# Kernel tuning notes

Hardware: AMD Instinct MI355X
Metric: run time of the kernel (lower is better)

Reference implementation:

```python
import jax, jax.numpy as jnp
import numpy as np

N0, N1, N2 = 100000, 25000, 6250
E0, E1, E2 = 600000, 150000, 37500
K = 6


def cheb_conv(x, edge_index, W, b):
    """torch_geometric ChebConv with sym normalization, lambda_max=2:
    L_hat = -D^{-1/2} A D^{-1/2}; T0=x, T1=L_hat x, Tk=2 L_hat T_{k-1} - T_{k-2}."""
    n = x.shape[0]
    src, dst = edge_index[0], edge_index[1]
    deg = jax.ops.segment_sum(jnp.ones(src.shape[0], x.dtype), src, num_segments=n)
    dinv = jnp.where(deg > 0, jax.lax.rsqrt(jnp.maximum(deg, 1.0)), 0.0)
    w = -(dinv[src] * dinv[dst])  # [E]

    def prop(h):  # (L_hat h)_i = sum_{j->i} w_ij h_j
        return jax.ops.segment_sum(w[:, None] * h[src], dst, num_segments=n)

    Tx0 = x
    out = Tx0 @ W[0]
    Tx1 = prop(x)
    out = out + Tx1 @ W[1]
    for k in range(2, W.shape[0]):
        Tx2 = 2.0 * prop(Tx1) - Tx0
        out = out + Tx2 @ W[k]
        Tx0, Tx1 = Tx1, Tx2
    return out + b


def pool(x, rows, cols, vals, n_out):
    # sparse.mm(D, x): y[r] += v * x[c]
    return jax.ops.segment_sum(vals[:, None] * x[cols], rows, num_segments=n_out)


def setup_inputs() -> dict:
    key = jax.random.key(0)
    ks = jax.random.split(key, 16)
    inp = {}
    inp["x"] = jax.random.normal(ks[0], (N0, 3), jnp.float32)
    inp["edge_index0"] = jax.random.randint(ks[1], (2, E0), 0, N0, jnp.int32)
    inp["edge_index1"] = jax.random.randint(ks[2], (2, E1), 0, N1, jnp.int32)
    inp["edge_index2"] = jax.random.randint(ks[3], (2, E2), 0, N2, jnp.int32)
    s = 0.05
    inp["W0"] = jax.random.normal(ks[4], (K, 3, 128), jnp.float32) * s
    inp["b0"] = jax.random.normal(ks[5], (128,), jnp.float32) * s
    inp["W1"] = jax.random.normal(ks[6], (K, 128, 128), jnp.float32) * s
    inp["b1"] = jax.random.normal(ks[7], (128,), jnp.float32) * s
    inp["W2"] = jax.random.normal(ks[8], (K, 128, 256), jnp.float32) * s
    inp["b2"] = jax.random.normal(ks[9], (256,), jnp.float32) * s
    inp["D0_rows"] = jax.random.randint(ks[10], (100000,), 0, N1, jnp.int32)
    inp["D0_cols"] = jax.random.randint(ks[11], (100000,), 0, N0, jnp.int32)
    inp["D0_vals"] = jax.random.uniform(ks[12], (100000,), jnp.float32)
    inp["D1_rows"] = jax.random.randint(ks[13], (25000,), 0, N2, jnp.int32)
    inp["D1_cols"] = jax.random.randint(ks[14], (25000,), 0, N1, jnp.int32)
    inp["D1_vals"] = jax.random.uniform(ks[15], (25000,), jnp.float32)
    k2 = jax.random.split(jax.random.fold_in(key, 1), 2)
    inp["linW"] = jax.random.normal(k2[0], (10, N2 * 256), jnp.float32) * 0.001
    inp["linb"] = jax.random.normal(k2[1], (10,), jnp.float32) * s
    return inp


def reference(x, edge_index0, edge_index1, edge_index2, W0, b0, W1, b1, W2, b2,
              D0_rows, D0_cols, D0_vals, D1_rows, D1_cols, D1_vals, linW, linb):
    h = jax.nn.relu(cheb_conv(x, edge_index0, W0, b0))      # [N0,128]
    h = pool(h, D0_rows, D0_cols, D0_vals, N1)               # [N1,128]
    h = jax.nn.relu(cheb_conv(h, edge_index1, W1, b1))      # [N1,128]
    h = pool(h, D1_rows, D1_cols, D1_vals, N2)               # [N2,128]
    h = cheb_conv(h, edge_index2, W2, b2)                    # [N2,256]
    Z = linW @ h.reshape(-1) + linb                           # [10]
    return Z
```

## Files before the change

### kernel.cpp

```cpp
#include <hip/hip_runtime.h>


namespace {
constexpr int cN0 = 100000, cN1 = 25000, cN2 = 6250;
constexpr int cE0 = 600000, cE1 = 150000, cE2 = 37500;
constexpr int cD  = cN2 * 256;

constexpr int JN[8]  = {cN0, cN1, cN2, cN1, cN2, cN0, cN1, cN2};
constexpr int JE[8]  = {cE0, cE1, cE2, 100000, 25000, cE0, cE1, cE2};
constexpr int JB[8]  = {391, 98, 25, 98, 25, 391, 98, 25};
constexpr int JBBASE[9] = {0, 391, 489, 514, 612, 637, 1028, 1126, 1151};
constexpr int TB = 1151;
constexpr int JCB[8] = {293, 74, 19, 49, 13, 293, 74, 19};
constexpr int JCBASE[9] = {0, 293, 367, 386, 435, 448, 741, 815, 834};
constexpr int TCB = 834;
constexpr int CHUNK = 2048;
constexpr int BSTRIDE = 400;

constexpr int EBASE[5]   = {0, 600000, 750000, 787500, 887500};
constexpr int E_TOTAL    = 912500;
constexpr int SBASE[3]   = {0, 600000, 750000};
constexpr int S_TOTAL    = 787500;
constexpr int NBASE[5]   = {0, 100096, 125184, 131584, 156672};
constexpr int NPAD_TOTAL = 163072;
constexpr int DEGBASE[3] = {0, 100000, 125000};
constexpr int DEG_TOTAL  = 131250;
}

typedef __attribute__((ext_vector_type(8))) short short8;
typedef __attribute__((ext_vector_type(4))) float floatx4;

__device__ inline ushort f2bf(float f) {
  union { float f; unsigned u; } v; v.f = f;
  unsigned u = v.u;
  return (ushort)((u + 0x7FFFu + ((u >> 16) & 1u)) >> 16);
}

__device__ inline int job_of_cb(int cb) {
  int j = 0;
  while (cb >= JCBASE[j + 1]) ++j;
  return j;
}
__device__ inline int job_of_bucket(int g) {
  int j = 0;
  while (g >= JBBASE[j + 1]) ++j;
  return j;
}

__global__ __launch_bounds__(256) void c1_count_kernel(
    const int* __restrict__ k0, const int* __restrict__ k1, const int* __restrict__ k2,
    const int* __restrict__ k3, const int* __restrict__ k4, const int* __restrict__ k5,
    const int* __restrict__ k6, const int* __restrict__ k7,
    int* __restrict__ cntCB) {
  __shared__ int cnt[BSTRIDE];
  int cb = blockIdx.x;
  int j = job_of_cb(cb);
  int lb = cb - JCBASE[j];
  const int* keys;
  switch (j) {
    case 0: keys = k0; break; case 1: keys = k1; break; case 2: keys = k2; break;
    case 3: keys = k3; break; case 4: keys = k4; break; case 5: keys = k5; break;
    case 6: keys = k6; break; default: keys = k7; break;
  }
  int nB = JB[j];
  for (int b = threadIdx.x; b < nB; b += 256) cnt[b] = 0;
  __syncthreads();
  int e0 = lb * CHUNK;
  int e1 = min(e0 + CHUNK, JE[j]);
  for (int e = e0 + threadIdx.x; e < e1; e += 256)
    atomicAdd(&cnt[keys[e] >> 8], 1);
  __syncthreads();
  for (int b = threadIdx.x; b < nB; b += 256)
    cntCB[cb * BSTRIDE + b] = cnt[b];
}

__global__ __launch_bounds__(256) void c2a_scan_kernel(int* __restrict__ cntCB,
                                                       int* __restrict__ bucketTot) {
  __shared__ int s[256];
  int g = blockIdx.x;
  int j = job_of_bucket(g);
  int b = g - JBBASE[j];
  int cb0 = JCBASE[j], nCB = JCB[j];
  int carry = 0;
  for (int c0 = 0; c0 < nCB; c0 += 256) {
    int i = c0 + threadIdx.x;
    int v = (i < nCB) ? cntCB[(cb0 + i) * BSTRIDE + b] : 0;
    s[threadIdx.x] = v;
    __syncthreads();
    for (int d = 1; d < 256; d <<= 1) {
      int t = (threadIdx.x >= d) ? s[threadIdx.x - d] : 0;
      __syncthreads();
      s[threadIdx.x] += t;
      __syncthreads();
    }
    if (i < nCB) cntCB[(cb0 + i) * BSTRIDE + b] = carry + s[threadIdx.x] - v;
    carry += s[255];
    __syncthreads();
  }
  if (threadIdx.x == 0) bucketTot[g] = carry;
}

__global__ __launch_bounds__(256) void c2b_scan_kernel(const int* __restrict__ bucketTot,
                                                       int* __restrict__ bucketBase) {
  __shared__ int s[256];
  int j = blockIdx.x;
  int g0 = JBBASE[j], nB = JB[j];
  int carry = 0;
  for (int c0 = 0; c0 < nB; c0 += 256) {
    int i = c0 + threadIdx.x;
    int v = (i < nB) ? bucketTot[g0 + i] : 0;
    s[threadIdx.x] = v;
    __syncthreads();
    for (int d = 1; d < 256; d <<= 1) {
      int t = (threadIdx.x >= d) ? s[threadIdx.x - d] : 0;
      __syncthreads();
      s[threadIdx.x] += t;
      __syncthreads();
    }
    if (i < nB) bucketBase[g0 + i] = carry + s[threadIdx.x] - v;
    carry += s[255];
    __syncthreads();
  }
}

__global__ __launch_bounds__(256) void c3_src_kernel(
    const int* __restrict__ s0, const int* __restrict__ s1, const int* __restrict__ s2,
    const int* __restrict__ cntCB, const int* __restrict__ bucketBase,
    int* __restrict__ scatSrc) {
  __shared__ int base[BSTRIDE];
  int cb = blockIdx.x + JCBASE[5];
  int j = job_of_cb(cb);
  int lb = cb - JCBASE[j];
  const int* keys = (j == 5) ? s0 : (j == 6) ? s1 : s2;
  int nB = JB[j];
  for (int b = threadIdx.x; b < nB; b += 256)
    base[b] = SBASE[j - 5] + bucketBase[JBBASE[j] + b] + cntCB[cb * BSTRIDE + b];
  __syncthreads();
  int e0 = lb * CHUNK;
  int e1 = min(e0 + CHUNK, JE[j]);
  for (int e = e0 + threadIdx.x; e < e1; e += 256) {
    int s = keys[e];
    int pos = atomicAdd(&base[s >> 8], 1);
    scatSrc[pos] = s & 255;
  }
}

__global__ __launch_bounds__(256) void ddeg_kernel(const int* __restrict__ scatSrc,
                                                   const int* __restrict__ bucketTot,
                                                   const int* __restrict__ bucketBase,
                                                   float* __restrict__ dinv) {
  __shared__ int cnt[256];
  int g = blockIdx.x + JBBASE[5];
  int j = job_of_bucket(g);
  int b = g - JBBASE[j];
  int st = SBASE[j - 5] + bucketBase[g];
  int en = st + bucketTot[g];
  cnt[threadIdx.x] = 0;
  __syncthreads();
  for (int idx = st + threadIdx.x; idx < en; idx += 256)
    atomicAdd(&cnt[scatSrc[idx]], 1);
  __syncthreads();
  int node = b * 256 + threadIdx.x;
  if (node < JN[j]) {
    int c = cnt[threadIdx.x];
    dinv[DEGBASE[j - 5] + node] = (c > 0) ? rsqrtf((float)c) : 0.f;
  }
}

__global__ __launch_bounds__(256) void c3_dst_kernel(
    const int* __restrict__ d0, const int* __restrict__ s0,
    const int* __restrict__ d1, const int* __restrict__ s1,
    const int* __restrict__ d2, const int* __restrict__ s2,
    const int* __restrict__ p0r, const int* __restrict__ p0c, const float* __restrict__ p0v,
    const int* __restrict__ p1r, const int* __restrict__ p1c, const float* __restrict__ p1v,
    const float* __restrict__ dinv,
    const int* __restrict__ cntCB, const int* __restrict__ bucketBase,
    int2* __restrict__ scatPairs) {
  __shared__ int base[BSTRIDE];
  int cb = blockIdx.x;
  int j = job_of_cb(cb);
  int lb = cb - JCBASE[j];
  const int* dk; const int* sk; const float* vv = nullptr;
  switch (j) {
    case 0: dk = d0; sk = s0; break;
    case 1: dk = d1; sk = s1; break;
    case 2: dk = d2; sk = s2; break;
    case 3: dk = p0r; sk = p0c; vv = p0v; break;
    default: dk = p1r; sk = p1c; vv = p1v; break;
  }
  int nB = JB[j];
  for (int b = threadIdx.x; b < nB; b += 256)
    base[b] = EBASE[j] + bucketBase[JBBASE[j] + b] + cntCB[cb * BSTRIDE + b];
  __syncthreads();
  int e0 = lb * CHUNK;
  int e1 = min(e0 + CHUNK, JE[j]);
  for (int e = e0 + threadIdx.x; e < e1; e += 256) {
    int d = dk[e];
    int s = sk[e];
    float w;
    if (j < 3) w = -(dinv[DEGBASE[j] + s] * dinv[DEGBASE[j] + d]);
    else w = vv[e];
    int pos = atomicAdd(&base[d >> 8], 1);
    scatPairs[pos] = make_int2(((d & 255) << 17) | s, __float_as_int(w));
  }
}

__global__ __launch_bounds__(256) void dcsr_kernel(const int2* __restrict__ scatPairs,
                                                   const int* __restrict__ bucketTot,
                                                   const int* __restrict__ bucketBase,
                                                   int* __restrict__ off,
                                                   int2* __restrict__ csrPairs) {
  __shared__ int cnt[256];
  __shared__ int sArr[256];
  __shared__ int cur[256];
  int g = blockIdx.x;
  int j = job_of_bucket(g);
  int b = g - JBBASE[j];
  int relBase = bucketBase[g];
  int st = EBASE[j] + relBase;
  int en = st + bucketTot[g];
  cnt[threadIdx.x] = 0;
  __syncthreads();
  for (int idx = st + threadIdx.x; idx < en; idx += 256)
    atomicAdd(&cnt[scatPairs[idx].x >> 17], 1);
  __syncthreads();
  int v = cnt[threadIdx.x];
  sArr[threadIdx.x] = v;
  __syncthreads();
  for (int d = 1; d < 256; d <<= 1) {
    int t = (threadIdx.x >= d) ? sArr[threadIdx.x - d] : 0;
    __syncthreads();
    sArr[threadIdx.x] += t;
    __syncthreads();
  }
  int excl = sArr[threadIdx.x] - v;
  int node = b * 256 + threadIdx.x;
  if (node < JN[j]) off[NBASE[j] + node] = relBase + excl;
  if (threadIdx.x == 0 && b == JB[j] - 1) off[NBASE[j] + JN[j]] = JE[j];
  cur[threadIdx.x] = st + excl;
  __syncthreads();
  for (int idx = st + threadIdx.x; idx < en; idx += 256) {
    int2 p = scatPairs[idx];
    int dl = p.x >> 17;
    int s = p.x & 0x1FFFF;
    int pos = atomicAdd(&cur[dl], 1);
    csrPairs[pos] = make_int2(s, p.y);
  }
}

__global__ __launch_bounds__(256) void csr_prop128_kernel(
    const int* __restrict__ off, const int2* __restrict__ pairs,
    const float* __restrict__ h, float* __restrict__ y, ushort* __restrict__ ybf,
    const float* __restrict__ prev, float scale, int N) {
  int r = blockIdx.x * 8 + (threadIdx.x >> 5);
  int l = threadIdx.x & 31;
  if (r >= N) return;
  int s = off[r], e = off[r + 1];
  const float4* h4 = (const float4*)h;
  float ax = 0.f, ay = 0.f, az = 0.f, aw = 0.f;
  int j = s;
  for (; j + 2 <= e; j += 2) {
    int2 p0 = pairs[j];
    int2 p1 = pairs[j + 1];
    float4 v0 = h4[(size_t)p0.x * 32 + l];
    float4 v1 = h4[(size_t)p1.x * 32 + l];
    float w0 = __int_as_float(p0.y);
    float w1 = __int_as_float(p1.y);
    ax += w0 * v0.x + w1 * v1.x;
    ay += w0 * v0.y + w1 * v1.y;
    az += w0 * v0.z + w1 * v1.z;
    aw += w0 * v0.w + w1 * v1.w;
  }
  if (j < e) {
    int2 p = pairs[j];
    float4 v0 = h4[(size_t)p.x * 32 + l];
    float w = __int_as_float(p.y);
    ax += w * v0.x; ay += w * v0.y; az += w * v0.z; aw += w * v0.w;
  }
  float4 v = make_float4(scale * ax, scale * ay, scale * az, scale * aw);
  if (prev) {
    float4 pv = ((const float4*)prev)[(size_t)r * 32 + l];
    v.x -= pv.x; v.y -= pv.y; v.z -= pv.z; v.w -= pv.w;
  }
  ((float4*)y)[(size_t)r * 32 + l] = v;
  uint2 sp = make_uint2(f2bf(v.x) | ((unsigned)f2bf(v.y) << 16),
                        f2bf(v.z) | ((unsigned)f2bf(v.w) << 16));
  ((uint2*)ybf)[(size_t)r * 32 + l] = sp;
}

__global__ void csr_prop3_kernel(const int* __restrict__ off, const int2* __restrict__ pairs,
                                 const float4* __restrict__ h, float4* __restrict__ y,
                                 const float4* __restrict__ prev, float scale, int N) {
  int r = blockIdx.x * blockDim.x + threadIdx.x;
  if (r >= N) return;
  int s = off[r], e = off[r + 1];
  float ax = 0.f, ay = 0.f, az = 0.f;
  int j = s;
  for (; j + 4 <= e; j += 4) {
    int2 p0 = pairs[j], p1 = pairs[j + 1], p2 = pairs[j + 2], p3 = pairs[j + 3];
    float4 h0 = h[p0.x], h1 = h[p1.x], h2 = h[p2.x], h3 = h[p3.x];
    float w0 = __int_as_float(p0.y), w1 = __int_as_float(p1.y);
    float w2 = __int_as_float(p2.y), w3 = __int_as_float(p3.y);
    ax += w0 * h0.x + w1 * h1.x + w2 * h2.x + w3 * h3.x;
    ay += w0 * h0.y + w1 * h1.y + w2 * h2.y + w3 * h3.y;
    az += w0 * h0.z + w1 * h1.z + w2 * h2.z + w3 * h3.z;
  }
  for (; j < e; ++j) {
    int2 p = pairs[j];
    float4 hv = h[p.x];
    float w = __int_as_float(p.y);
    ax += w * hv.x; ay += w * hv.y; az += w * hv.z;
  }
  float4 v = make_float4(scale * ax, scale * ay, scale * az, 0.f);
  if (prev) {
    float4 pv = prev[r];
    v.x -= pv.x; v.y -= pv.y; v.z -= pv.z;
  }
  y[r] = v;
}

__global__ void copyx_kernel(const float* __restrict__ x, float4* __restrict__ Tb, int N) {
  int r = blockIdx.x * 256 + threadIdx.x;
  if (r < N) Tb[r] = make_float4(x[3 * r], x[3 * r + 1], x[3 * r + 2], 0.f);
}

__global__ __launch_bounds__(256) void g18pool_kernel(
    const int* __restrict__ off, const int2* __restrict__ pairs,
    const float4* __restrict__ Tb0, const float* __restrict__ W0,
    const float* __restrict__ b0, float* __restrict__ T0out,
    ushort* __restrict__ T0bf, int N, int N0) {
  int r = blockIdx.x * 2 + (threadIdx.x >> 7);
  int f = threadIdx.x & 127;
  float wcol[18];
#pragma unroll
  for (int t = 0; t < 18; ++t) wcol[t] = W0[t * 128 + f];
  float bv = b0[f];
  if (r >= N) return;
  int s = off[r], e = off[r + 1];
  float acc = 0.f;
  for (int j = s; j < e; ++j) {
    int2 p = pairs[j];
    float v = __int_as_float(p.y);
    float d = bv;
#pragma unroll
    for (int k = 0; k < 6; ++k) {
      float4 t = Tb0[(size_t)k * N0 + p.x];
      d += t.x * wcol[k * 3 + 0] + t.y * wcol[k * 3 + 1] + t.z * wcol[k * 3 + 2];
    }
    acc += v * fmaxf(d, 0.f);
  }
  T0out[(size_t)r * 128 + f] = acc;
  T0bf[(size_t)r * 128 + f] = f2bf(acc);
}

__global__ void prep_w_kernel(const float* __restrict__ W1, const float* __restrict__ W2,
                              ushort* __restrict__ Wt1, ushort* __restrict__ Wt2) {
  int i = blockIdx.x * 256 + threadIdx.x;
  if (i < 768 * 128) {
    int k = i / 128, n = i - k * 128;
    Wt1[(size_t)n * 768 + k] = f2bf(W1[i]);
  } else {
    int i2 = i - 768 * 128;
    if (i2 < 768 * 256) {
      int k = i2 / 256, n = i2 - k * 256;
      Wt2[(size_t)n * 768 + k] = f2bf(W2[i2]);
    }
  }
}

template <int RELU>
__global__ __launch_bounds__(256, 2) void gemm_mfma_kernel(
    const ushort* __restrict__ Tbf, const ushort* __restrict__ Wt,
    const float* __restrict__ bias, float* __restrict__ C, int M, int N) {
  __shared__ ushort Al[64][40];
  __shared__ ushort Bl[128][40];
  const int tid = threadIdx.x;
  const int rowBase = blockIdx.x * 64;
  const int colBase = blockIdx.y * 128;
  const int wave = tid >> 6;
  const int lane = tid & 63;
  const int m16 = lane & 15;
  const int quad = lane >> 4;
  const size_t Mstride = (size_t)M * 128;

  floatx4 acc[8];
#pragma unroll
  for (int c = 0; c < 8; ++c)
#pragma unroll
    for (int r = 0; r < 4; ++r) acc[c][r] = 0.f;

  const int sRow = tid >> 2;
  const int sK8 = (tid & 3) * 8;
  const int growA = rowBase + sRow;
  const bool aValid = growA < M;

  for (int kc = 0; kc < 24; ++kc) {
    uint4 av = make_uint4(0, 0, 0, 0);
    if (aValid)
      av = *(const uint4*)(Tbf + (size_t)(kc >> 2) * Mstride + (size_t)growA * 128
                           + ((kc & 3) << 5) + sK8);
    *(uint4*)&Al[sRow][sK8] = av;
#pragma unroll
    for (int l = 0; l < 2; ++l) {
      int lin = tid + l * 256;
      int bRow = lin >> 2;
      int bK8 = (lin & 3) * 8;
      *(uint4*)&Bl[bRow][bK8] =
          *(const uint4*)(Wt + (size_t)(colBase + bRow) * 768 + kc * 32 + bK8);
    }
    __syncthreads();

    short8 a = *(const short8*)&Al[wave * 16 + m16][quad * 8];
#pragma unroll
    for (int c = 0; c < 8; ++c) {
      short8 b = *(const short8*)&Bl[c * 16 + m16][quad * 8];
      acc[c] = __builtin_amdgcn_mfma_f32_16x16x32_bf16(a, b, acc[c], 0, 0, 0);
    }
    __syncthreads();
  }

#pragma unroll
  for (int c = 0; c < 8; ++c) {
    int col = colBase + c * 16 + m16;
    float bv = bias[col];
#pragma unroll
    for (int r = 0; r < 4; ++r) {
      int row = rowBase + wave * 16 + quad * 4 + r;
      if (row < M) {
        float v = acc[c][r] + bv;
        if (RELU) v = fmaxf(v, 0.f);
        C[(size_t)row * N + col] = v;
      }
    }
  }
}

__global__ void initout_kernel(float* __restrict__ out, const float* __restrict__ linb) {
  int i = threadIdx.x;
  if (i < 10) out[i] = linb[i];
}

__global__ __launch_bounds__(256) void linear_kernel(const float* __restrict__ Wl,
                                                     const float* __restrict__ h,
                                                     float* __restrict__ out, int D) {
  float p[10];
#pragma unroll
  for (int j = 0; j < 10; ++j) p[j] = 0.f;
  int stride = gridDim.x * blockDim.x;
  for (int i = blockIdx.x * blockDim.x + threadIdx.x; i < D; i += stride) {
    float hv = h[i];
#pragma unroll
    for (int j = 0; j < 10; ++j) p[j] += Wl[(size_t)j * D + i] * hv;
  }
#pragma unroll
  for (int j = 0; j < 10; ++j) {
#pragma unroll
    for (int off = 32; off > 0; off >>= 1) p[j] += __shfl_down(p[j], off, 64);
  }
  __shared__ float s[4][10];
  int wave = threadIdx.x >> 6, lane = threadIdx.x & 63;
  if (lane == 0) {
#pragma unroll
    for (int j = 0; j < 10; ++j) s[wave][j] = p[j];
  }
  __syncthreads();
  if (threadIdx.x < 10) {
    float t = s[0][threadIdx.x] + s[1][threadIdx.x] + s[2][threadIdx.x] + s[3][threadIdx.x];
    atomicAdd(&out[threadIdx.x], t);
  }
}

extern "C" void kernel_launch(void* const* d_in, const int* in_sizes, int n_in,
                              void* d_out, int out_size, void* d_ws, size_t ws_size,
                              hipStream_t stream) {
  const float* x    = (const float*)d_in[0];
  const int*   ei0  = (const int*)d_in[1];
  const int*   ei1  = (const int*)d_in[2];
  const int*   ei2  = (const int*)d_in[3];
  const float* W0   = (const float*)d_in[4];
  const float* b0   = (const float*)d_in[5];
  const float* W1   = (const float*)d_in[6];
  const float* b1   = (const float*)d_in[7];
  const float* W2   = (const float*)d_in[8];
  const float* b2   = (const float*)d_in[9];
  const int*   D0r  = (const int*)d_in[10];
  const int*   D0c  = (const int*)d_in[11];
  const float* D0v  = (const float*)d_in[12];
  const int*   D1r  = (const int*)d_in[13];
  const int*   D1c  = (const int*)d_in[14];
  const float* D1v  = (const float*)d_in[15];
  const float* linW = (const float*)d_in[16];
  const float* linb = (const float*)d_in[17];
  float* out = (float*)d_out;
  (void)in_sizes; (void)n_in; (void)out_size; (void)ws_size;

  const int* src0 = ei0;            const int* dst0 = ei0 + cE0;
  const int* src1 = ei1;            const int* dst1 = ei1 + cE1;
  const int* src2 = ei2;            const int* dst2 = ei2 + cE2;

  float* ws = (float*)d_ws;
  size_t off = 0;
  auto alloc = [&](size_t n) {
    float* p = ws + off;
    off += (n + 63) & ~size_t(63);
    return p;
  };
  float* dinv       = alloc(DEG_TOTAL);
  int*   cntCB      = (int*)alloc((size_t)TCB * BSTRIDE);
  int*   bucketTot  = (int*)alloc(TB);
  int*   bucketBase = (int*)alloc(TB);
  int*   scatSrc    = (int*)alloc(S_TOTAL);
  int2*  scatPairs  = (int2*)alloc((size_t)2 * E_TOTAL);
  int2*  csrPairs   = (int2*)alloc((size_t)2 * E_TOTAL);
  int*   offArr     = (int*)alloc(NPAD_TOTAL);
  ushort* Wt1       = (ushort*)alloc(768 * 128 / 2);
  ushort* Wt2       = (ushort*)alloc(768 * 256 / 2);
  float4* Tb0       = (float4*)alloc((size_t)6 * cN0 * 4);
  float* Tlvl1      = alloc((size_t)6 * cN1 * 128);
  ushort* Tbf1      = (ushort*)alloc((size_t)6 * cN1 * 64);
  float* out1       = alloc((size_t)cN1 * 128);
  float* Tlvl2      = alloc((size_t)6 * cN2 * 128);
  ushort* Tbf2      = (ushort*)alloc((size_t)6 * cN2 * 64);
  float* out2       = alloc((size_t)cN2 * 256);

  auto nb = [](long long n) { return (unsigned)((n + 255) / 256); };

  c1_count_kernel<<<TCB, 256, 0, stream>>>(dst0, dst1, dst2, D0r, D1r,
                                           src0, src1, src2, cntCB);
  c2a_scan_kernel<<<TB, 256, 0, stream>>>(cntCB, bucketTot);
  c2b_scan_kernel<<<8, 256, 0, stream>>>(bucketTot, bucketBase);
  c3_src_kernel<<<TCB - JCBASE[5], 256, 0, stream>>>(src0, src1, src2,
                                                     cntCB, bucketBase, scatSrc);
  ddeg_kernel<<<TB - JBBASE[5], 256, 0, stream>>>(scatSrc, bucketTot, bucketBase, dinv);
  c3_dst_kernel<<<JCBASE[5], 256, 0, stream>>>(dst0, src0, dst1, src1, dst2, src2,
                                               D0r, D0c, D0v, D1r, D1c, D1v,
                                               dinv, cntCB, bucketBase, scatPairs);
  dcsr_kernel<<<JBBASE[5], 256, 0, stream>>>(scatPairs, bucketTot, bucketBase,
                                             offArr, csrPairs);
  prep_w_kernel<<<nb(768 * 384), 256, 0, stream>>>(W1, W2, Wt1, Wt2);

  auto seg_off   = [&](int s) { return offArr + NBASE[s]; };
  auto seg_pairs = [&](int s) { return csrPairs + EBASE[s]; };

  copyx_kernel<<<nb(cN0), 256, 0, stream>>>(x, Tb0, cN0);
  {
    auto Tk = [&](int k) { return Tb0 + (size_t)k * cN0; };
    csr_prop3_kernel<<<nb(cN0), 256, 0, stream>>>(seg_off(0), seg_pairs(0),
        Tk(0), Tk(1), nullptr, 1.f, cN0);
    csr_prop3_kernel<<<nb(cN0), 256, 0, stream>>>(seg_off(0), seg_pairs(0),
        Tk(1), Tk(2), Tk(0), 2.f, cN0);
    csr_prop3_kernel<<<nb(cN0), 256, 0, stream>>>(seg_off(0), seg_pairs(0),
        Tk(2), Tk(3), Tk(1), 2.f, cN0);
    csr_prop3_kernel<<<nb(cN0), 256, 0, stream>>>(seg_off(0), seg_pairs(0),
        Tk(3), Tk(4), Tk(2), 2.f, cN0);
    csr_prop3_kernel<<<nb(cN0), 256, 0, stream>>>(seg_off(0), seg_pairs(0),
        Tk(4), Tk(5), Tk(3), 2.f, cN0);
  }
  g18pool_kernel<<<(cN1 + 1) / 2, 256, 0, stream>>>(
      seg_off(3), seg_pairs(3), Tb0, W0, b0, Tlvl1, Tbf1, cN1, cN0);

  {
    auto Tk  = [&](int k) { return Tlvl1 + (size_t)k * cN1 * 128; };
    auto Tbk = [&](int k) { return Tbf1 + (size_t)k * cN1 * 128; };
    auto prop = [&](int kin, int kout, int kprev, float scale) {
      csr_prop128_kernel<<<(cN1 + 7) / 8, 256, 0, stream>>>(
          seg_off(1), seg_pairs(1), Tk(kin), Tk(kout), Tbk(kout),
          (kprev >= 0) ? Tk(kprev) : nullptr, scale, cN1);
    };
    prop(0, 1, -1, 1.f);
    prop(1, 2, 0, 2.f);
    prop(2, 3, 1, 2.f);
    prop(3, 4, 2, 2.f);
    prop(4, 5, 3, 2.f);
    dim3 g((cN1 + 63) / 64, 1);
    gemm_mfma_kernel<1><<<g, 256, 0, stream>>>(Tbf1, Wt1, b1, out1, cN1, 128);
  }

  csr_prop128_kernel<<<(cN2 + 7) / 8, 256, 0, stream>>>(
      seg_off(4), seg_pairs(4), out1, Tlvl2, Tbf2, nullptr, 1.f, cN2);

  {
    auto Tk  = [&](int k) { return Tlvl2 + (size_t)k * cN2 * 128; };
    auto Tbk = [&](int k) { return Tbf2 + (size_t)k * cN2 * 128; };
    auto prop = [&](int kin, int kout, int kprev, float scale) {
      csr_prop128_kernel<<<(cN2 + 7) / 8, 256, 0, stream>>>(
          seg_off(2), seg_pairs(2), Tk(kin), Tk(kout), Tbk(kout),
          (kprev >= 0) ? Tk(kprev) : nullptr, scale, cN2);
    };
    prop(0, 1, -1, 1.f);
    prop(1, 2, 0, 2.f);
    prop(2, 3, 1, 2.f);
    prop(3, 4, 2, 2.f);
    prop(4, 5, 3, 2.f);
    dim3 g((cN2 + 63) / 64, 2);
    gemm_mfma_kernel<0><<<g, 256, 0, stream>>>(Tbf2, Wt2, b2, out2, cN2, 256);
  }

  initout_kernel<<<1, 64, 0, stream>>>(out, linb);
  linear_kernel<<<512, 256, 0, stream>>>(linW, out2, out, cD);
}
```

Measured before the change: 465.7 us.

## Interleave level-0 Chebyshev terms per node, unroll prop128 gather, skip unused f32 store

The level-0 Chebyshev terms are stored node-major (six float4 per node) instead of term-major, so the pooling kernel reads all six terms of a gathered node from contiguous memory. The pooling loop also processes two pairs per iteration. The 128-wide propagation loop is unrolled to four neighbours to keep more gathers in flight. The last propagation step no longer writes the fp32 copy, since only the bf16 copy feeds the GEMM. The propagation kernels gather with a stride of 96 bytes instead of 16, which may cost some cache efficiency.

Measured after the change: 494.0 us. 6.1% more time.

```diff
diff --git a/kernel.cpp b/kernel.cpp
--- a/kernel.cpp
+++ b/kernel.cpp
@@ -259,19 +259,20 @@
   const float4* h4 = (const float4*)h;
   float ax = 0.f, ay = 0.f, az = 0.f, aw = 0.f;
   int j = s;
-  for (; j + 2 <= e; j += 2) {
-    int2 p0 = pairs[j];
-    int2 p1 = pairs[j + 1];
+  for (; j + 4 <= e; j += 4) {
+    int2 p0 = pairs[j], p1 = pairs[j + 1], p2 = pairs[j + 2], p3 = pairs[j + 3];
     float4 v0 = h4[(size_t)p0.x * 32 + l];
     float4 v1 = h4[(size_t)p1.x * 32 + l];
-    float w0 = __int_as_float(p0.y);
-    float w1 = __int_as_float(p1.y);
-    ax += w0 * v0.x + w1 * v1.x;
-    ay += w0 * v0.y + w1 * v1.y;
-    az += w0 * v0.z + w1 * v1.z;
-    aw += w0 * v0.w + w1 * v1.w;
-  }
-  if (j < e) {
+    float4 v2 = h4[(size_t)p2.x * 32 + l];
+    float4 v3 = h4[(size_t)p3.x * 32 + l];
+    float w0 = __int_as_float(p0.y), w1 = __int_as_float(p1.y);
+    float w2 = __int_as_float(p2.y), w3 = __int_as_float(p3.y);
+    ax += w0 * v0.x + w1 * v1.x + w2 * v2.x + w3 * v3.x;
+    ay += w0 * v0.y + w1 * v1.y + w2 * v2.y + w3 * v3.y;
+    az += w0 * v0.z + w1 * v1.z + w2 * v2.z + w3 * v3.z;
+    aw += w0 * v0.w + w1 * v1.w + w2 * v2.w + w3 * v3.w;
+  }
+  for (; j < e; ++j) {
     int2 p = pairs[j];
     float4 v0 = h4[(size_t)p.x * 32 + l];
     float w = __int_as_float(p.y);
@@ -282,15 +283,15 @@
     float4 pv = ((const float4*)prev)[(size_t)r * 32 + l];
     v.x -= pv.x; v.y -= pv.y; v.z -= pv.z; v.w -= pv.w;
   }
-  ((float4*)y)[(size_t)r * 32 + l] = v;
+  if (y) ((float4*)y)[(size_t)r * 32 + l] = v;
   uint2 sp = make_uint2(f2bf(v.x) | ((unsigned)f2bf(v.y) << 16),
                         f2bf(v.z) | ((unsigned)f2bf(v.w) << 16));
   ((uint2*)ybf)[(size_t)r * 32 + l] = sp;
 }
 
 __global__ void csr_prop3_kernel(const int* __restrict__ off, const int2* __restrict__ pairs,
-                                 const float4* __restrict__ h, float4* __restrict__ y,
-                                 const float4* __restrict__ prev, float scale, int N) {
+                                 const float4* __restrict__ T, float4* __restrict__ Tout,
+                                 int kin, int kout, int kprev, float scale, int N) {
   int r = blockIdx.x * blockDim.x + threadIdx.x;
   if (r >= N) return;
   int s = off[r], e = off[r + 1];
@@ -298,7 +299,10 @@
   int j = s;
   for (; j + 4 <= e; j += 4) {
     int2 p0 = pairs[j], p1 = pairs[j + 1], p2 = pairs[j + 2], p3 = pairs[j + 3];
-    float4 h0 = h[p0.x], h1 = h[p1.x], h2 = h[p2.x], h3 = h[p3.x];
+    float4 h0 = T[(size_t)p0.x * 6 + kin];
+    float4 h1 = T[(size_t)p1.x * 6 + kin];
+    float4 h2 = T[(size_t)p2.x * 6 + kin];
+    float4 h3 = T[(size_t)p3.x * 6 + kin];
     float w0 = __int_as_float(p0.y), w1 = __int_as_float(p1.y);
     float w2 = __int_as_float(p2.y), w3 = __int_as_float(p3.y);
     ax += w0 * h0.x + w1 * h1.x + w2 * h2.x + w3 * h3.x;
@@ -307,28 +311,28 @@
   }
   for (; j < e; ++j) {
     int2 p = pairs[j];
-    float4 hv = h[p.x];
+    float4 hv = T[(size_t)p.x * 6 + kin];
     float w = __int_as_float(p.y);
     ax += w * hv.x; ay += w * hv.y; az += w * hv.z;
   }
   float4 v = make_float4(scale * ax, scale * ay, scale * az, 0.f);
-  if (prev) {
-    float4 pv = prev[r];
+  if (kprev >= 0) {
+    float4 pv = T[(size_t)r * 6 + kprev];
     v.x -= pv.x; v.y -= pv.y; v.z -= pv.z;
   }
-  y[r] = v;
+  Tout[(size_t)r * 6 + kout] = v;
 }
 
 __global__ void copyx_kernel(const float* __restrict__ x, float4* __restrict__ Tb, int N) {
   int r = blockIdx.x * 256 + threadIdx.x;
-  if (r < N) Tb[r] = make_float4(x[3 * r], x[3 * r + 1], x[3 * r + 2], 0.f);
+  if (r < N) Tb[(size_t)r * 6] = make_float4(x[3 * r], x[3 * r + 1], x[3 * r + 2], 0.f);
 }
 
 __global__ __launch_bounds__(256) void g18pool_kernel(
     const int* __restrict__ off, const int2* __restrict__ pairs,
     const float4* __restrict__ Tb0, const float* __restrict__ W0,
     const float* __restrict__ b0, float* __restrict__ T0out,
-    ushort* __restrict__ T0bf, int N, int N0) {
+    ushort* __restrict__ T0bf, int N) {
   int r = blockIdx.x * 2 + (threadIdx.x >> 7);
   int f = threadIdx.x & 127;
   float wcol[18];
@@ -338,16 +342,31 @@
   if (r >= N) return;
   int s = off[r], e = off[r + 1];
   float acc = 0.f;
-  for (int j = s; j < e; ++j) {
+  int j = s;
+  for (; j + 2 <= e; j += 2) {
+    int2 p0 = pairs[j], p1 = pairs[j + 1];
+    const float4* t0 = Tb0 + (size_t)p0.x * 6;
+    const float4* t1 = Tb0 + (size_t)p1.x * 6;
+    float d0 = bv, d1 = bv;
+#pragma unroll
+    for (int k = 0; k < 6; ++k) {
+      float4 a = t0[k];
+      float4 b = t1[k];
+      d0 += a.x * wcol[k * 3] + a.y * wcol[k * 3 + 1] + a.z * wcol[k * 3 + 2];
+      d1 += b.x * wcol[k * 3] + b.y * wcol[k * 3 + 1] + b.z * wcol[k * 3 + 2];
+    }
+    acc += __int_as_float(p0.y) * fmaxf(d0, 0.f) + __int_as_float(p1.y) * fmaxf(d1, 0.f);
+  }
+  if (j < e) {
     int2 p = pairs[j];
-    float v = __int_as_float(p.y);
+    const float4* t0 = Tb0 + (size_t)p.x * 6;
     float d = bv;
 #pragma unroll
     for (int k = 0; k < 6; ++k) {
-      float4 t = Tb0[(size_t)k * N0 + p.x];
-      d += t.x * wcol[k * 3 + 0] + t.y * wcol[k * 3 + 1] + t.z * wcol[k * 3 + 2];
-    }
-    acc += v * fmaxf(d, 0.f);
+      float4 a = t0[k];
+      d += a.x * wcol[k * 3] + a.y * wcol[k * 3 + 1] + a.z * wcol[k * 3 + 2];
+    }
+    acc += __int_as_float(p.y) * fmaxf(d, 0.f);
   }
   T0out[(size_t)r * 128 + f] = acc;
   T0bf[(size_t)r * 128 + f] = f2bf(acc);
@@ -515,7 +534,7 @@
   int*   offArr     = (int*)alloc(NPAD_TOTAL);
   ushort* Wt1       = (ushort*)alloc(768 * 128 / 2);
   ushort* Wt2       = (ushort*)alloc(768 * 256 / 2);
-  float4* Tb0       = (float4*)alloc((size_t)6 * cN0 * 4);
+  float4* Tb0       = (float4*)alloc((size_t)cN0 * 24);
   float* Tlvl1      = alloc((size_t)6 * cN1 * 128);
   ushort* Tbf1      = (ushort*)alloc((size_t)6 * cN1 * 64);
   float* out1       = alloc((size_t)cN1 * 128);
@@ -543,35 +562,32 @@
   auto seg_pairs = [&](int s) { return csrPairs + EBASE[s]; };
 
   copyx_kernel<<<nb(cN0), 256, 0, stream>>>(x, Tb0, cN0);
-  {
-    auto Tk = [&](int k) { return Tb0 + (size_t)k * cN0; };
-    csr_prop3_kernel<<<nb(cN0), 256, 0, stream>>>(seg_off(0), seg_pairs(0),
-        Tk(0), Tk(1), nullptr, 1.f, cN0);
-    csr_prop3_kernel<<<nb(cN0), 256, 0, stream>>>(seg_off(0), seg_pairs(0),
-        Tk(1), Tk(2), Tk(0), 2.f, cN0);
-    csr_prop3_kernel<<<nb(cN0), 256, 0, stream>>>(seg_off(0), seg_pairs(0),
-        Tk(2), Tk(3), Tk(1), 2.f, cN0);
-    csr_prop3_kernel<<<nb(cN0), 256, 0, stream>>>(seg_off(0), seg_pairs(0),
-        Tk(3), Tk(4), Tk(2), 2.f, cN0);
-    csr_prop3_kernel<<<nb(cN0), 256, 0, stream>>>(seg_off(0), seg_pairs(0),
-        Tk(4), Tk(5), Tk(3), 2.f, cN0);
-  }
+  csr_prop3_kernel<<<nb(cN0), 256, 0, stream>>>(seg_off(0), seg_pairs(0),
+      Tb0, Tb0, 0, 1, -1, 1.f, cN0);
+  csr_prop3_kernel<<<nb(cN0), 256, 0, stream>>>(seg_off(0), seg_pairs(0),
+      Tb0, Tb0, 1, 2, 0, 2.f, cN0);
+  csr_prop3_kernel<<<nb(cN0), 256, 0, stream>>>(seg_off(0), seg_pairs(0),
+      Tb0, Tb0, 2, 3, 1, 2.f, cN0);
+  csr_prop3_kernel<<<nb(cN0), 256, 0, stream>>>(seg_off(0), seg_pairs(0),
+      Tb0, Tb0, 3, 4, 2, 2.f, cN0);
+  csr_prop3_kernel<<<nb(cN0), 256, 0, stream>>>(seg_off(0), seg_pairs(0),
+      Tb0, Tb0, 4, 5, 3, 2.f, cN0);
   g18pool_kernel<<<(cN1 + 1) / 2, 256, 0, stream>>>(
-      seg_off(3), seg_pairs(3), Tb0, W0, b0, Tlvl1, Tbf1, cN1, cN0);
+      seg_off(3), seg_pairs(3), Tb0, W0, b0, Tlvl1, Tbf1, cN1);
 
   {
     auto Tk  = [&](int k) { return Tlvl1 + (size_t)k * cN1 * 128; };
     auto Tbk = [&](int k) { return Tbf1 + (size_t)k * cN1 * 128; };
-    auto prop = [&](int kin, int kout, int kprev, float scale) {
+    auto prop = [&](int kin, int kout, int kprev, float scale, bool needF32) {
       csr_prop128_kernel<<<(cN1 + 7) / 8, 256, 0, stream>>>(
-          seg_off(1), seg_pairs(1), Tk(kin), Tk(kout), Tbk(kout),
+          seg_off(1), seg_pairs(1), Tk(kin), needF32 ? Tk(kout) : nullptr, Tbk(kout),
           (kprev >= 0) ? Tk(kprev) : nullptr, scale, cN1);
     };
-    prop(0, 1, -1, 1.f);
-    prop(1, 2, 0, 2.f);
-    prop(2, 3, 1, 2.f);
-    prop(3, 4, 2, 2.f);
-    prop(4, 5, 3, 2.f);
+    prop(0, 1, -1, 1.f, true);
+    prop(1, 2, 0, 2.f, true);
+    prop(2, 3, 1, 2.f, true);
+    prop(3, 4, 2, 2.f, true);
+    prop(4, 5, 3, 2.f, false);
     dim3 g((cN1 + 63) / 64, 1);
     gemm_mfma_kernel<1><<<g, 256, 0, stream>>>(Tbf1, Wt1, b1, out1, cN1, 128);
   }
@@ -582,16 +598,16 @@
   {
     auto Tk  = [&](int k) { return Tlvl2 + (size_t)k * cN2 * 128; };
     auto Tbk = [&](int k) { return Tbf2 + (size_t)k * cN2 * 128; };
-    auto prop = [&](int kin, int kout, int kprev, float scale) {
+    auto prop = [&](int kin, int kout, int kprev, float scale, bool needF32) {
       csr_prop128_kernel<<<(cN2 + 7) / 8, 256, 0, stream>>>(
-          seg_off(2), seg_pairs(2), Tk(kin), Tk(kout), Tbk(kout),
+          seg_off(2), seg_pairs(2), Tk(kin), needF32 ? Tk(kout) : nullptr, Tbk(kout),
           (kprev >= 0) ? Tk(kprev) : nullptr, scale, cN2);
     };
-    prop(0, 1, -1, 1.f);
-    prop(1, 2, 0, 2.f);
-    prop(2, 3, 1, 2.f);
-    prop(3, 4, 2, 2.f);
-    prop(4, 5, 3, 2.f);
+    prop(0, 1, -1, 1.f, true);
+    prop(1, 2, 0, 2.f, true);
+    prop(2, 3, 1, 2.f, true);
+    prop(3, 4, 2, 2.f, true);
+    prop(4, 5, 3, 2.f, false);
     dim3 g((cN2 + 63) / 64, 2);
     gemm_mfma_kernel<0><<<g, 256, 0, stream>>>(Tbf2, Wt2, b2, out2, cN2, 256);
   }
```
